# Performance work log

Hardware: AMD Instinct MI355X
Metric: run time of the kernel (lower is better)

The kernel has to match this reference:

```python
import jax, jax.numpy as jnp
import numpy as np

WS = 7        # window_size
HEADS = 4     # dim_in // dim_head = 256 // 64
DH = 64       # dim_head (for q/k)
SCALE = DH ** -0.5


def setup_inputs() -> dict:
    key = jax.random.key(0)
    k1, k2, k3 = jax.random.split(key, 3)
    x = jax.random.normal(k1, (32, 256, 56, 56), dtype=jnp.float32)
    qk_w = jax.random.normal(k2, (512, 256), dtype=jnp.float32) * 0.02  # 1x1 conv: (out_c, in_c)
    v_w = jax.random.normal(k3, (256, 256), dtype=jnp.float32) * 0.02
    return {"x": x, "qk_w": qk_w, "v_w": v_w}


def _forward(x, qk_w, v_w):
    B, C, H, W = x.shape
    pad_b = (WS - H % WS) % WS
    pad_r = (WS - W % WS) % WS
    x = jnp.pad(x, ((0, 0), (0, 0), (0, pad_b), (0, pad_r)))
    Hp, Wp = H + pad_b, W + pad_r
    n1, n2 = Hp // WS, Wp // WS

    # 1x1 convs (no bias): qk -> 2*C channels, v -> dim_mid channels with ReLU
    qk = jnp.einsum('bchw,oc->bohw', x, qk_w)
    v = jax.nn.relu(jnp.einsum('bchw,oc->bohw', x, v_w))

    # remote (dilated grid) partition: 'b c (h1 n1) (w1 n2) -> (b n1 n2) c h1 w1'
    def part_r(t):
        b, c = t.shape[:2]
        return t.reshape(b, c, WS, n1, WS, n2).transpose(0, 3, 5, 1, 2, 4).reshape(b * n1 * n2, c, WS, WS)

    def merge_r(t, b):
        c = t.shape[1]
        return t.reshape(b, n1, n2, c, WS, WS).transpose(0, 3, 4, 1, 5, 2).reshape(b, c, Hp, Wp)

    # close (contiguous window) partition: 'b c (n1 h1) (n2 w1) -> (b n1 n2) c h1 w1'
    def part_c(t):
        b, c = t.shape[:2]
        return t.reshape(b, c, n1, WS, n2, WS).transpose(0, 2, 4, 1, 3, 5).reshape(b * n1 * n2, c, WS, WS)

    def merge_c(t, b):
        c = t.shape[1]
        return t.reshape(b, n1, n2, c, WS, WS).transpose(0, 3, 1, 4, 2, 5).reshape(b, c, Hp, Wp)

    def win_attn(qk_win, v_win):
        # qk_win: (bw, 2*HEADS*DH, WS, WS); channel order is (qk, heads, dim_head)
        bw = qk_win.shape[0]
        N = WS * WS
        qkr = qk_win.reshape(bw, 2, HEADS, DH, N)
        q = qkr[:, 0].transpose(0, 1, 3, 2)  # (bw, heads, N, DH)
        k = qkr[:, 1].transpose(0, 1, 3, 2)
        dhv = v_win.shape[1] // HEADS
        vv = v_win.reshape(bw, HEADS, dhv, N).transpose(0, 1, 3, 2)  # (bw, heads, N, dhv)
        attn = jax.nn.softmax(jnp.einsum('bhnd,bhmd->bhnm', q, k) * SCALE, axis=-1)
        o = jnp.einsum('bhnm,bhmd->bhnd', attn, vv)
        return o.transpose(0, 1, 3, 2).reshape(bw, HEADS * dhv, WS, WS)

    o_remote = merge_r(win_attn(part_r(qk), part_r(v)), B)
    o_close = merge_c(win_attn(part_c(qk), part_c(v)), B)
    out = o_remote + o_close
    return out[:, :, :H, :W]


def reference(x, qk_w, v_w):
    return _forward(x, qk_w, v_w)
```

## Files before the change

kernel.cpp:

```cpp
#include <hip/hip_runtime.h>
#include <stdint.h>


typedef float f32x4 __attribute__((ext_vector_type(4)));
typedef __attribute__((ext_vector_type(8))) short short8;

union V16 { uint4 u; short8 s; unsigned short h[8]; };

typedef const __attribute__((address_space(1))) uint32_t* gp_t;
typedef __attribute__((address_space(3))) uint32_t* lp_t;

__device__ __forceinline__ void async16(const void* g, void* l) {
  __builtin_amdgcn_global_load_lds((gp_t)g, (lp_t)l, 16, 0, 0);
}

__device__ __forceinline__ unsigned short f2bf(float f) {
  union { float f; uint32_t u; } a; a.f = f;
  uint32_t u = a.u;
  return (unsigned short)((u + 0x7FFFu + ((u >> 16) & 1u)) >> 16);
}

__device__ __forceinline__ unsigned short f2bf_rhu(float f) {
  union { float f; uint32_t u; } a; a.f = f;
  return (unsigned short)((a.u + 0x8000u) >> 16);
}

__device__ __forceinline__ float bf2f(uint32_t bits_hi16) {
  union { uint32_t u; float f; } a; a.u = bits_hi16; return a.f;
}

__global__ __launch_bounds__(256) void k_wconv(const float* __restrict__ qk_w,
                                               const float* __restrict__ v_w,
                                               unsigned short* __restrict__ Wb) {
  int i = blockIdx.x * 256 + threadIdx.x;
  int o = i >> 5, gidx = i & 31;
  int c0 = gidx * 8;
  const float* src = (o < 512) ? (qk_w + o * 256 + c0) : (v_w + (o - 512) * 256 + c0);
  unsigned short vv[8];
#pragma unroll
  for (int j = 0; j < 8; j++) vv[j] = f2bf(src[j]);
  uint4 u;
  u.x = (uint32_t)vv[0] | ((uint32_t)vv[1] << 16);
  u.y = (uint32_t)vv[2] | ((uint32_t)vv[3] << 16);
  u.z = (uint32_t)vv[4] | ((uint32_t)vv[5] << 16);
  u.w = (uint32_t)vv[6] | ((uint32_t)vv[7] << 16);
  int kb = gidx >> 3, gg = gidx & 7;
  char* dst = (char*)Wb + (size_t)o * 512 + kb * 128 + ((gg ^ (o & 7)) << 4);
  *(uint4*)dst = u;
}

__global__ __launch_bounds__(256) void k_xpose(const float* __restrict__ x,
                                               unsigned short* __restrict__ xT) {
  const int t = threadIdx.x;
  const int p = blockIdx.x * 64 + (t >> 2);
  const int sub = t & 3;
  const int c0 = blockIdx.y * 32 + sub * 8;
  const int b = blockIdx.z;
  const float* xp = x + ((size_t)(b * 256 + c0)) * 3136 + p;
  unsigned short vv[8];
#pragma unroll
  for (int j = 0; j < 8; j++) vv[j] = f2bf(xp[(size_t)j * 3136]);
  uint4 u;
  u.x = (uint32_t)vv[0] | ((uint32_t)vv[1] << 16);
  u.y = (uint32_t)vv[2] | ((uint32_t)vv[3] << 16);
  u.z = (uint32_t)vv[4] | ((uint32_t)vv[5] << 16);
  u.w = (uint32_t)vv[6] | ((uint32_t)vv[7] << 16);
  const int g = (c0 >> 3) & 7;
  const int kb = c0 >> 6;
  char* dst = (char*)xT + ((size_t)(b * 3136 + p)) * 512 + kb * 128 + ((g ^ (p & 7)) << 4);
  *(uint4*)dst = u;
}

__global__ __launch_bounds__(256) void k_conv(const unsigned short* __restrict__ Wb,
                                              const unsigned short* __restrict__ xT,
                                              unsigned short* __restrict__ qkv) {
  __shared__ uint4 lds4[4096];
  char* lds = (char*)lds4;
  const int bi = blockIdx.x;
  const int xcd = bi & 7, g = bi >> 3;
  const int bgrp = g / 150;
  const int rem = g - bgrp * 150;
  const int b = xcd + 8 * bgrp;
  const int ot = rem / 25;
  const int pt = rem - ot * 25;
  const int p0 = pt * 128, o0 = ot * 128;
  const bool isv = (ot >= 4);
  const float qs = (ot < 2) ? 0.18033688011112042f : 1.0f;

  const int tid = threadIdx.x;
  const int lane = tid & 63, wave = tid >> 6;
  const int lid = lane & 15, quad = lane >> 4;
  const int m_off = (wave & 1) * 64, n_off = (wave >> 1) * 64;
  const int psub = lane >> 3, chunk = lane & 7;
  const size_t rowb = (size_t)(b * 3136 + p0);
  const char* xTb = (const char*)xT;
  const char* Wbb = (const char*)Wb;

  auto stage = [&](int kk, char* buf) {
    char* ldsA = buf;
    char* ldsB = buf + 16384;
#pragma unroll
    for (int r = 0; r < 4; r++) {
      int i = wave * 4 + r;
      const char* ga = Wbb + (size_t)(o0 + i * 8 + psub) * 512 + kk * 2 + chunk * 16;
      async16(ga, ldsA + i * 1024);
      const char* gb = xTb + (rowb + i * 8 + psub) * 512 + kk * 2 + chunk * 16;
      async16(gb, ldsB + i * 1024);
    }
  };

  f32x4 acc[4][4];
#pragma unroll
  for (int mi = 0; mi < 4; mi++)
#pragma unroll
    for (int ni = 0; ni < 4; ni++) { f32x4 z = {0.f, 0.f, 0.f, 0.f}; acc[mi][ni] = z; }

  stage(0, lds);
  asm volatile("s_waitcnt vmcnt(0)" ::: "memory");
  __builtin_amdgcn_s_barrier();

#pragma unroll
  for (int t = 0; t < 4; t++) {
    char* cur = lds + (t & 1) * 32768;
    if (t < 3) stage((t + 1) * 64, lds + ((t + 1) & 1) * 32768);
    char* ldsA = cur;
    char* ldsB = cur + 16384;

    V16 a[4][2], bf[4][2];
#pragma unroll
    for (int mi = 0; mi < 4; mi++) {
      int ro = m_off + mi * 16 + lid;
#pragma unroll
      for (int ks = 0; ks < 2; ks++) {
        int gl = ks * 4 + quad;
        a[mi][ks].u = *(const uint4*)(ldsA + ro * 128 + ((gl ^ (ro & 7)) << 4));
      }
    }
#pragma unroll
    for (int ni = 0; ni < 4; ni++) {
      int px = n_off + ni * 16 + lid;
#pragma unroll
      for (int ks = 0; ks < 2; ks++) {
        int gl = ks * 4 + quad;
        bf[ni][ks].u = *(const uint4*)(ldsB + px * 128 + ((gl ^ (px & 7)) << 4));
      }
    }
#pragma unroll
    for (int mi = 0; mi < 4; mi++)
#pragma unroll
      for (int ni = 0; ni < 4; ni++) {
        acc[mi][ni] = __builtin_amdgcn_mfma_f32_16x16x32_bf16(a[mi][0].s, bf[ni][0].s, acc[mi][ni], 0, 0, 0);
        acc[mi][ni] = __builtin_amdgcn_mfma_f32_16x16x32_bf16(a[mi][1].s, bf[ni][1].s, acc[mi][ni], 0, 0, 0);
      }

    asm volatile("s_waitcnt vmcnt(0)" ::: "memory");
    __builtin_amdgcn_s_barrier();
  }

#pragma unroll
  for (int mi = 0; mi < 4; mi++) {
    const int chunkb = (m_off >> 3) + mi * 2 + (quad >> 1);
#pragma unroll
    for (int ni = 0; ni < 4; ni++) {
      const int pxl = n_off + ni * 16 + lid;
      f32x4 v = acc[mi][ni];
      v.x *= qs; v.y *= qs; v.z *= qs; v.w *= qs;
      if (isv) {
        v.x = fmaxf(v.x, 0.f); v.y = fmaxf(v.y, 0.f);
        v.z = fmaxf(v.z, 0.f); v.w = fmaxf(v.w, 0.f);
      }
      uint32_t lo = (uint32_t)f2bf(v.x) | ((uint32_t)f2bf(v.y) << 16);
      uint32_t hi = (uint32_t)f2bf(v.z) | ((uint32_t)f2bf(v.w) << 16);
      uint2 st; st.x = lo; st.y = hi;
      *(uint2*)(lds + pxl * 256 + ((chunkb ^ (pxl & 7)) << 4) + (quad & 1) * 8) = st;
    }
  }
  __syncthreads();

#pragma unroll
  for (int rep = 0; rep < 8; rep++) {
    int idx = rep * 256 + tid;
    int pxl = idx >> 4, seg = idx & 15;
    uint4 vv = *(const uint4*)(lds + pxl * 256 + ((seg ^ (pxl & 7)) << 4));
    int px = p0 + pxl;
    if (px < 3136)
      *(uint4*)((char*)qkv + ((size_t)(b * 3136 + px)) * 1536 + o0 * 2 + seg * 16) = vv;
  }
}

template <int PART, int FUSED>
__global__ __launch_bounds__(256) void k_attn_t(const unsigned short* __restrict__ qkv,
                                                const unsigned short* __restrict__ oPrev,
                                                unsigned short* __restrict__ oDst,
                                                float* __restrict__ out) {
  __shared__ uint4 smem4[2048];
  const int bi = blockIdx.x;
  const int xcd = bi & 7, g = bi >> 3;
  const int b = ((g >> 6) << 3) + xcd;
  const int w = g & 63;
  const int i1 = w >> 3, i2 = w & 7;
  const int off = PART ? (i1 * 392 + i2 * 7) : (i1 * 56 + i2);
  const int sh  = PART ? 56 : 448;
  const int sw  = PART ? 1 : 8;

  const int lane = threadIdx.x & 63;
  const int head = threadIdx.x >> 6;
  const int lid = lane & 15, quad = lane >> 4;
  char* Pb = (char*)smem4 + head * 8192;
  const unsigned short* __restrict__ qkvb = qkv + (size_t)b * 3136 * 768;

  auto pix = [&](int t) -> int {
    int h1 = (t * 37) >> 8;
    int w1 = t - h1 * 7;
    return off + h1 * sh + w1 * sw;
  };

  V16 va[4][2];
#pragma unroll
  for (int ks = 0; ks < 2; ks++)
#pragma unroll
    for (int j = 0; j < 8; j++) {
      int key = ks * 32 + quad * 8 + j;
      int p = pix(min(key, 48));
      const unsigned short* vp = qkvb + p * 768 + 512 + head * 64 + lid;
#pragma unroll
      for (int mi = 0; mi < 4; mi++) va[mi][ks].h[j] = vp[mi * 16];
    }

  V16 qf[4][2], kf[4][2];
#pragma unroll
  for (int mi = 0; mi < 4; mi++) {
    int p = pix(min(mi * 16 + lid, 48));
    const unsigned short* qp = qkvb + p * 768 + head * 64;
#pragma unroll
    for (int ks = 0; ks < 2; ks++) qf[mi][ks].u = *(const uint4*)(qp + ks * 32 + quad * 8);
  }
#pragma unroll
  for (int ni = 0; ni < 4; ni++) {
    int p = pix(min(ni * 16 + lid, 48));
    const unsigned short* kp = qkvb + p * 768 + 256 + head * 64;
#pragma unroll
    for (int ks = 0; ks < 2; ks++) kf[ni][ks].u = *(const uint4*)(kp + ks * 32 + quad * 8);
  }

  f32x4 s[4][4];
#pragma unroll
  for (int mi = 0; mi < 4; mi++)
#pragma unroll
    for (int ni = 0; ni < 4; ni++) {
      f32x4 z = {0.f, 0.f, 0.f, 0.f};
      z = __builtin_amdgcn_mfma_f32_16x16x32_bf16(kf[mi][0].s, qf[ni][0].s, z, 0, 0, 0);
      z = __builtin_amdgcn_mfma_f32_16x16x32_bf16(kf[mi][1].s, qf[ni][1].s, z, 0, 0, 0);
      s[mi][ni] = z;
    }

  {
    const int rx = lid & 7;
    char* wbase = Pb + lid * 128 + (quad & 1) * 8;
#pragma unroll
    for (int mi = 0; mi < 4; mi++) {
      const int swz = ((mi * 2 + (quad >> 1)) ^ rx) << 4;
#pragma unroll
      for (int ni = 0; ni < 4; ni++) {
        uint32_t d0, d1;
        if (mi < 3) {
          d0 = (uint32_t)f2bf_rhu(__builtin_amdgcn_exp2f(s[mi][ni][0]))
             | ((uint32_t)f2bf_rhu(__builtin_amdgcn_exp2f(s[mi][ni][1])) << 16);
          d1 = (uint32_t)f2bf_rhu(__builtin_amdgcn_exp2f(s[mi][ni][2]))
             | ((uint32_t)f2bf_rhu(__builtin_amdgcn_exp2f(s[mi][ni][3])) << 16);
        } else {
          d0 = quad ? 0u : (uint32_t)f2bf_rhu(__builtin_amdgcn_exp2f(s[3][ni][0]));
          d1 = 0u;
        }
        uint2 st; st.x = d0; st.y = d1;
        *(uint2*)(wbase + ni * 2048 + swz) = st;
      }
    }
  }
  __syncthreads();

  V16 pt[4][2];
#pragma unroll
  for (int ni = 0; ni < 4; ni++) {
    int row = ni * 16 + lid;
#pragma unroll
    for (int ks = 0; ks < 2; ks++) {
      int gl = ks * 4 + quad;
      pt[ni][ks].u = *(const uint4*)(Pb + row * 128 + ((gl ^ (row & 7)) << 4));
    }
  }

  V16 ones;
#pragma unroll
  for (int j = 0; j < 8; j++) ones.h[j] = 0x3F80;
  float inv[4];
  int pq[4]; bool qv[4];
#pragma unroll
  for (int ni = 0; ni < 4; ni++) {
    f32x4 z = {0.f, 0.f, 0.f, 0.f};
    z = __builtin_amdgcn_mfma_f32_16x16x32_bf16(ones.s, pt[ni][0].s, z, 0, 0, 0);
    z = __builtin_amdgcn_mfma_f32_16x16x32_bf16(ones.s, pt[ni][1].s, z, 0, 0, 0);
    inv[ni] = __builtin_amdgcn_rcpf(z[0]);
    int q = ni * 16 + lid;
    qv[ni] = q < 49;
    pq[ni] = pix(qv[ni] ? q : 48);
  }

#pragma unroll
  for (int mi = 0; mi < 4; mi++) {
    f32x4 om[4];
#pragma unroll
    for (int ni = 0; ni < 4; ni++) {
      f32x4 z = {0.f, 0.f, 0.f, 0.f};
      z = __builtin_amdgcn_mfma_f32_16x16x32_bf16(va[mi][0].s, pt[ni][0].s, z, 0, 0, 0);
      z = __builtin_amdgcn_mfma_f32_16x16x32_bf16(va[mi][1].s, pt[ni][1].s, z, 0, 0, 0);
      om[ni] = z;
    }
    if constexpr (!FUSED) {
      unsigned short* __restrict__ oSb = oDst + (size_t)b * 3136 * 256;
#pragma unroll
      for (int ni = 0; ni < 4; ni++) {
        if (qv[ni]) {
          float iv = inv[ni];
          uint32_t lo = ((uint32_t)f2bf_rhu(om[ni][0] * iv)) | ((uint32_t)f2bf_rhu(om[ni][1] * iv) << 16);
          uint32_t hi = ((uint32_t)f2bf_rhu(om[ni][2] * iv)) | ((uint32_t)f2bf_rhu(om[ni][3] * iv) << 16);
          uint2 st; st.x = lo; st.y = hi;
          *(uint2*)(oSb + pq[ni] * 256 + head * 64 + mi * 16 + quad * 4) = st;
        }
      }
    } else {
      const unsigned short* __restrict__ oPb = oPrev + (size_t)b * 3136 * 256;
      float* __restrict__ outb = out + (size_t)b * 256 * 3136;
      const int c0 = head * 64 + mi * 16 + quad * 4;
#pragma unroll
      for (int ni = 0; ni < 4; ni++) {
        if (qv[ni]) {
          float iv = inv[ni];
          uint2 r = *(const uint2*)(oPb + pq[ni] * 256 + c0);
          float o0 = om[ni][0] * iv + bf2f(r.x << 16);
          float o1 = om[ni][1] * iv + bf2f(r.x & 0xFFFF0000u);
          float o2 = om[ni][2] * iv + bf2f(r.y << 16);
          float o3 = om[ni][3] * iv + bf2f(r.y & 0xFFFF0000u);
          float* op = outb + (size_t)c0 * 3136 + pq[ni];
          op[0]        = o0;
          op[3136]     = o1;
          op[2 * 3136] = o2;
          op[3 * 3136] = o3;
        }
      }
    }
  }
}

extern "C" void kernel_launch(void* const* d_in, const int* in_sizes, int n_in,
                              void* d_out, int out_size, void* d_ws, size_t ws_size,
                              hipStream_t stream) {
  (void)in_sizes; (void)n_in; (void)out_size; (void)ws_size;
  const float* x    = (const float*)d_in[0];
  const float* qk_w = (const float*)d_in[1];
  const float* v_w  = (const float*)d_in[2];
  float* out = (float*)d_out;
  char* ws = (char*)d_ws;
  unsigned short* Wb  = (unsigned short*)ws;
  unsigned short* xT  = (unsigned short*)(ws + 393216);
  unsigned short* qkv = (unsigned short*)(ws + 51773440ull);
  unsigned short* oR  = xT;

  hipLaunchKernelGGL(k_wconv, dim3(96), dim3(256), 0, stream, qk_w, v_w, Wb);
  hipLaunchKernelGGL(k_xpose, dim3(49, 8, 32), dim3(256), 0, stream, x, xT);
  hipLaunchKernelGGL(k_conv, dim3(4800), dim3(256), 0, stream, Wb, xT, qkv);
  hipLaunchKernelGGL(HIP_KERNEL_NAME(k_attn_t<0, 0>), dim3(2048), dim3(256), 0, stream,
                     qkv, (const unsigned short*)nullptr, oR, (float*)nullptr);
  hipLaunchKernelGGL(HIP_KERNEL_NAME(k_attn_t<1, 1>), dim3(2048), dim3(256), 0, stream,
                     qkv, (const unsigned short*)oR, (unsigned short*)nullptr, out);
}
```

Baseline: 361.2 us.

## Load conv GEMM operands directly from global memory instead of LDS staging

```diff
diff --git a/kernel.cpp b/kernel.cpp
--- a/kernel.cpp
+++ b/kernel.cpp
@@ -6,13 +6,6 @@
 typedef __attribute__((ext_vector_type(8))) short short8;
 
 union V16 { uint4 u; short8 s; unsigned short h[8]; };
-
-typedef const __attribute__((address_space(1))) uint32_t* gp_t;
-typedef __attribute__((address_space(3))) uint32_t* lp_t;
-
-__device__ __forceinline__ void async16(const void* g, void* l) {
-  __builtin_amdgcn_global_load_lds((gp_t)g, (lp_t)l, 16, 0, 0);
-}
 
 __device__ __forceinline__ unsigned short f2bf(float f) {
   union { float f; uint32_t u; } a; a.f = f;
@@ -44,9 +37,7 @@
   u.y = (uint32_t)vv[2] | ((uint32_t)vv[3] << 16);
   u.z = (uint32_t)vv[4] | ((uint32_t)vv[5] << 16);
   u.w = (uint32_t)vv[6] | ((uint32_t)vv[7] << 16);
-  int kb = gidx >> 3, gg = gidx & 7;
-  char* dst = (char*)Wb + (size_t)o * 512 + kb * 128 + ((gg ^ (o & 7)) << 4);
-  *(uint4*)dst = u;
+  *(uint4*)(Wb + (size_t)o * 256 + c0) = u;
 }
 
 __global__ __launch_bounds__(256) void k_xpose(const float* __restrict__ x,
@@ -65,16 +56,13 @@
   u.y = (uint32_t)vv[2] | ((uint32_t)vv[3] << 16);
   u.z = (uint32_t)vv[4] | ((uint32_t)vv[5] << 16);
   u.w = (uint32_t)vv[6] | ((uint32_t)vv[7] << 16);
-  const int g = (c0 >> 3) & 7;
-  const int kb = c0 >> 6;
-  char* dst = (char*)xT + ((size_t)(b * 3136 + p)) * 512 + kb * 128 + ((g ^ (p & 7)) << 4);
-  *(uint4*)dst = u;
+  *(uint4*)(xT + ((size_t)(b * 3136 + p)) * 256 + c0) = u;
 }
 
 __global__ __launch_bounds__(256) void k_conv(const unsigned short* __restrict__ Wb,
                                               const unsigned short* __restrict__ xT,
                                               unsigned short* __restrict__ qkv) {
-  __shared__ uint4 lds4[4096];
+  __shared__ uint4 lds4[2048];
   char* lds = (char*)lds4;
   const int bi = blockIdx.x;
   const int xcd = bi & 7, g = bi >> 3;
@@ -91,23 +79,16 @@
   const int lane = tid & 63, wave = tid >> 6;
   const int lid = lane & 15, quad = lane >> 4;
   const int m_off = (wave & 1) * 64, n_off = (wave >> 1) * 64;
-  const int psub = lane >> 3, chunk = lane & 7;
   const size_t rowb = (size_t)(b * 3136 + p0);
-  const char* xTb = (const char*)xT;
-  const char* Wbb = (const char*)Wb;
-
-  auto stage = [&](int kk, char* buf) {
-    char* ldsA = buf;
-    char* ldsB = buf + 16384;
-#pragma unroll
-    for (int r = 0; r < 4; r++) {
-      int i = wave * 4 + r;
-      const char* ga = Wbb + (size_t)(o0 + i * 8 + psub) * 512 + kk * 2 + chunk * 16;
-      async16(ga, ldsA + i * 1024);
-      const char* gb = xTb + (rowb + i * 8 + psub) * 512 + kk * 2 + chunk * 16;
-      async16(gb, ldsB + i * 1024);
-    }
-  };
+
+  const char* baseA[4];
+  const char* baseB[4];
+#pragma unroll
+  for (int mi = 0; mi < 4; mi++)
+    baseA[mi] = (const char*)Wb + (size_t)(o0 + m_off + mi * 16 + lid) * 512 + quad * 16;
+#pragma unroll
+  for (int ni = 0; ni < 4; ni++)
+    baseB[ni] = (const char*)xT + (rowb + n_off + ni * 16 + lid) * 512 + quad * 16;
 
   f32x4 acc[4][4];
 #pragma unroll
@@ -115,46 +96,26 @@
 #pragma unroll
     for (int ni = 0; ni < 4; ni++) { f32x4 z = {0.f, 0.f, 0.f, 0.f}; acc[mi][ni] = z; }
 
-  stage(0, lds);
-  asm volatile("s_waitcnt vmcnt(0)" ::: "memory");
-  __builtin_amdgcn_s_barrier();
-
 #pragma unroll
   for (int t = 0; t < 4; t++) {
-    char* cur = lds + (t & 1) * 32768;
-    if (t < 3) stage((t + 1) * 64, lds + ((t + 1) & 1) * 32768);
-    char* ldsA = cur;
-    char* ldsB = cur + 16384;
-
-    V16 a[4][2], bf[4][2];
-#pragma unroll
-    for (int mi = 0; mi < 4; mi++) {
-      int ro = m_off + mi * 16 + lid;
-#pragma unroll
-      for (int ks = 0; ks < 2; ks++) {
-        int gl = ks * 4 + quad;
-        a[mi][ks].u = *(const uint4*)(ldsA + ro * 128 + ((gl ^ (ro & 7)) << 4));
-      }
-    }
-#pragma unroll
-    for (int ni = 0; ni < 4; ni++) {
-      int px = n_off + ni * 16 + lid;
-#pragma unroll
-      for (int ks = 0; ks < 2; ks++) {
-        int gl = ks * 4 + quad;
-        bf[ni][ks].u = *(const uint4*)(ldsB + px * 128 + ((gl ^ (px & 7)) << 4));
-      }
-    }
+    V16 a[4][2], bv[4][2];
 #pragma unroll
     for (int mi = 0; mi < 4; mi++)
 #pragma unroll
+      for (int ks = 0; ks < 2; ks++)
+        a[mi][ks].u = *(const uint4*)(baseA[mi] + t * 128 + ks * 64);
+#pragma unroll
+    for (int ni = 0; ni < 4; ni++)
+#pragma unroll
+      for (int ks = 0; ks < 2; ks++)
+        bv[ni][ks].u = *(const uint4*)(baseB[ni] + t * 128 + ks * 64);
+#pragma unroll
+    for (int mi = 0; mi < 4; mi++)
+#pragma unroll
       for (int ni = 0; ni < 4; ni++) {
-        acc[mi][ni] = __builtin_amdgcn_mfma_f32_16x16x32_bf16(a[mi][0].s, bf[ni][0].s, acc[mi][ni], 0, 0, 0);
-        acc[mi][ni] = __builtin_amdgcn_mfma_f32_16x16x32_bf16(a[mi][1].s, bf[ni][1].s, acc[mi][ni], 0, 0, 0);
-      }
-
-    asm volatile("s_waitcnt vmcnt(0)" ::: "memory");
-    __builtin_amdgcn_s_barrier();
+        acc[mi][ni] = __builtin_amdgcn_mfma_f32_16x16x32_bf16(a[mi][0].s, bv[ni][0].s, acc[mi][ni], 0, 0, 0);
+        acc[mi][ni] = __builtin_amdgcn_mfma_f32_16x16x32_bf16(a[mi][1].s, bv[ni][1].s, acc[mi][ni], 0, 0, 0);
+      }
   }
 
 #pragma unroll
```

Measured after the change: 452.0 us. +25.1%, slower.
